# Performance work log

Measured on AMD Instinct MI355X. Metric: run time of the kernel, lower is better.

## Reference

```python
import jax, jax.numpy as jnp
import numpy as np

B, T_FRAMES, C, WS = 8, 8, 32, 128
N = 1024            # sample_size^2 points per frame
HW = WS * WS        # 16384 grid cells
BT = B * T_FRAMES


def setup_inputs() -> dict:
    key = jax.random.key(0)
    k1, k2, k3 = jax.random.split(key, 3)
    rng = np.random.default_rng(0)
    # per-frame grid-cell id for each of N points
    pose = rng.integers(0, HW, size=(BT, N))
    sorted_indices = np.argsort(pose, axis=1).astype(np.int32)
    sorted_pose = np.take_along_axis(pose, sorted_indices, axis=1)
    seq_unique_list = np.zeros((BT, N), dtype=np.int32)
    seq_unique_counts = np.zeros((BT, N), dtype=np.int32)
    for i in range(BT):
        u, c = np.unique(sorted_pose[i], return_counts=True)
        seq_unique_list[i, : len(u)] = u
        seq_unique_counts[i, : len(u)] = c
    return {
        "w_part": jax.random.normal(k1, (BT, N, C), dtype=jnp.float32),
        "sorted_indices": jnp.asarray(sorted_indices),
        "seq_unique_list": jnp.asarray(seq_unique_list),
        "seq_unique_counts": jnp.asarray(seq_unique_counts),
        "past_w": jax.random.normal(k2, (B, C, WS, WS), dtype=jnp.float32),
        "past_w_num_mask": jax.random.uniform(k3, (B, 1, WS, WS), dtype=jnp.float32) * 4.0,
        "T": T_FRAMES,
    }


def reference(w_part, sorted_indices, seq_unique_list, seq_unique_counts, past_w, past_w_num_mask, T):
    bt, n, c = w_part.shape
    b = bt // T
    ws = past_w.shape[2]
    hw = ws * ws
    # F.normalize(dim=-1), eps=1e-12
    wp = w_part / jnp.maximum(jnp.linalg.norm(w_part, axis=-1, keepdims=True), 1e-12)
    # gather: reorder points so same-cell points are contiguous
    gathered = jnp.take_along_axis(wp, sorted_indices[..., None].astype(jnp.int32), axis=1)  # (bt, n, c)
    counts = seq_unique_counts  # (bt, n) padded with zeros
    # segment id of each point from cumulative counts (points are sorted by cell)
    cum = jnp.cumsum(counts, axis=1)
    pt = jnp.arange(n)
    seg = jax.vmap(lambda cu: jnp.searchsorted(cu, pt, side='right'))(cum)  # (bt, n)
    sums = jax.vmap(lambda g, s: jax.ops.segment_sum(g, s, num_segments=n))(gathered, seg)  # (bt, n, c)
    means = sums / jnp.maximum(counts, 1)[..., None].astype(wp.dtype)
    # scatter means into dense grid; padded (count==0) slots routed out-of-bounds and dropped
    idx = jnp.where(counts > 0, seq_unique_list, hw)
    scat = jax.vmap(lambda m, i: jnp.zeros((hw, c), wp.dtype).at[i].set(m, mode='drop'))(means, idx)  # (bt, hw, c)
    mask = jax.vmap(lambda ct, i: jnp.zeros((hw,), wp.dtype).at[i].set(ct.astype(wp.dtype), mode='drop'))(counts, idx)
    new_w = scat.reshape(b, T, hw, c).mean(axis=1)                 # (b, hw, c)
    new_w = new_w.transpose(0, 2, 1).reshape(b, c, ws, ws)          # (b, c, ws, ws)
    w_num_mask = mask.reshape(b, T, hw).sum(axis=1).reshape(b, 1, ws, ws)
    # merge with past map; denominator is detached in the original
    new_w_num_mask = jax.lax.stop_gradient(w_num_mask) + jax.lax.stop_gradient(past_w_num_mask)
    new_w_num_mask = jnp.where(new_w_num_mask == 0, 1.0, new_w_num_mask)
    w = (new_w * w_num_mask + past_w * past_w_num_mask) / new_w_num_mask
    return w, new_w_num_mask
```

## Files before the change

kernel.cpp:

```cpp
#include <hip/hip_runtime.h>
#include <climits>

#define BATCH   8
#define TFRAMES 8
#define BT      (BATCH * TFRAMES)
#define NPTS    1024
#define NCH     32
#define WS      128
#define HW      (WS * WS)
#define CELLS   128
#define CHUNKS  (HW / CELLS)
#define CPAD    33

__global__ __launch_bounds__(256) void scan_kernel(
    const int* __restrict__ uniq_cnt,
    const int* __restrict__ uniq_list,
    int*       __restrict__ starts,
    int*       __restrict__ ranges)
{
    __shared__ int s_tot[256];
    __shared__ int s_key[NPTS];
    const int tid = threadIdx.x;
    const int bt  = blockIdx.x;

    const int4 c4 = reinterpret_cast<const int4*>(uniq_cnt + bt * NPTS)[tid];
    const int4 l4 = reinterpret_cast<const int4*>(uniq_list + bt * NPTS)[tid];
    s_key[tid * 4 + 0] = (c4.x > 0) ? l4.x : INT_MAX;
    s_key[tid * 4 + 1] = (c4.y > 0) ? l4.y : INT_MAX;
    s_key[tid * 4 + 2] = (c4.z > 0) ? l4.z : INT_MAX;
    s_key[tid * 4 + 3] = (c4.w > 0) ? l4.w : INT_MAX;

    const int l0 = c4.x;
    const int l1 = l0 + c4.y;
    const int l2 = l1 + c4.z;
    const int l3 = l2 + c4.w;
    s_tot[tid] = l3;
    __syncthreads();
    for (int off = 1; off < 256; off <<= 1) {
        int v = (tid >= off) ? s_tot[tid - off] : 0;
        __syncthreads();
        s_tot[tid] += v;
        __syncthreads();
    }
    const int ex = (tid > 0) ? s_tot[tid - 1] : 0;
    int4 st;
    st.x = ex;
    st.y = ex + l0;
    st.z = ex + l1;
    st.w = ex + l2;
    reinterpret_cast<int4*>(starts + bt * NPTS)[tid] = st;

    if (tid <= CHUNKS) {
        const int X = tid * CELLS;
        int lo = 0, hi = NPTS;
        while (lo < hi) {
            const int mid = (lo + hi) >> 1;
            if (s_key[mid] < X) lo = mid + 1; else hi = mid;
        }
        ranges[bt * (CHUNKS + 1) + tid] = lo;
    }
}

__global__ __launch_bounds__(256) void tile_kernel(
    const float* __restrict__ w_part,
    const int*   __restrict__ sorted_idx,
    const int*   __restrict__ uniq_list,
    const int*   __restrict__ uniq_cnt,
    const int*   __restrict__ starts,
    const int*   __restrict__ ranges,
    const float* __restrict__ past_w,
    const float* __restrict__ past_mask,
    float*       __restrict__ out_w,
    float*       __restrict__ out_mask)
{
    __shared__ float s_acc[CELLS][CPAD];
    __shared__ float s_mask[CELLS];

    const int tid      = threadIdx.x;
    const int b        = blockIdx.x / CHUNKS;
    const int chunk    = blockIdx.x % CHUNKS;
    const int cellBase = chunk * CELLS;

    float* flat = &s_acc[0][0];
    for (int i = tid; i < CELLS * CPAD; i += 256) flat[i] = 0.0f;
    if (tid < CELLS) s_mask[tid] = 0.0f;
    __syncthreads();

    const int wave  = tid >> 6;
    const int lane  = tid & 63;
    const int slot  = lane >> 3;
    const int lane8 = lane & 7;

    for (int tt = 0; tt < 2; ++tt) {
        const int t  = wave * 2 + tt;
        const int bt = b * TFRAMES + t;
        const int lo = ranges[bt * (CHUNKS + 1) + chunk];
        const int hi = ranges[bt * (CHUNKS + 1) + chunk + 1];
        const int* __restrict__ lst  = uniq_list + bt * NPTS;
        const int* __restrict__ cnts = uniq_cnt + bt * NPTS;
        const int* __restrict__ stp  = starts + bt * NPTS;
        const int* __restrict__ si   = sorted_idx + bt * NPTS;

        for (int e0 = lo; e0 < hi; e0 += 8) {
            const int e = e0 + slot;
            if (e < hi) {
                const int cell  = lst[e];
                const int cnt   = cnts[e];
                const int start = stp[e];
                float4 lacc = make_float4(0.f, 0.f, 0.f, 0.f);
                for (int p = start; p < start + cnt; ++p) {
                    const int j = si[p];
                    const float4 v = *reinterpret_cast<const float4*>(
                        w_part + ((size_t)bt * NPTS + j) * NCH + lane8 * 4);
                    float ss = v.x * v.x + v.y * v.y + v.z * v.z + v.w * v.w;
                    ss += __shfl_xor(ss, 1);
                    ss += __shfl_xor(ss, 2);
                    ss += __shfl_xor(ss, 4);
                    const float scale = 1.0f / fmaxf(sqrtf(ss), 1e-12f);
                    lacc.x += v.x * scale;
                    lacc.y += v.y * scale;
                    lacc.z += v.z * scale;
                    lacc.w += v.w * scale;
                }
                const float invc = 1.0f / (float)cnt;
                const int cl = cell - cellBase;
                float* ap = &s_acc[cl][lane8 * 4];
                atomicAdd(ap + 0, lacc.x * invc);
                atomicAdd(ap + 1, lacc.y * invc);
                atomicAdd(ap + 2, lacc.z * invc);
                atomicAdd(ap + 3, lacc.w * invc);
                if (lane8 == 0) atomicAdd(&s_mask[cl], (float)cnt);
            }
        }
    }
    __syncthreads();

    const int cellq = tid & 31;
    const int cgrp  = tid >> 5;
    const int c0    = cgrp * 4;
    const int gc    = cellBase + cellq * 4;
    const float invT = 1.0f / (float)TFRAMES;

    const float4 pm4 = *reinterpret_cast<const float4*>(past_mask + (size_t)b * HW + gc);
    float m[4], pm[4], r[4], dn[4];
    pm[0] = pm4.x; pm[1] = pm4.y; pm[2] = pm4.z; pm[3] = pm4.w;
#pragma unroll
    for (int i = 0; i < 4; ++i) {
        m[i] = s_mask[cellq * 4 + i];
        const float nwm = m[i] + pm[i];
        dn[i] = (nwm == 0.0f) ? 1.0f : nwm;
        r[i] = 1.0f / dn[i];
    }
    if (cgrp == 0) {
        float4 d4 = make_float4(dn[0], dn[1], dn[2], dn[3]);
        *reinterpret_cast<float4*>(out_mask + (size_t)b * HW + gc) = d4;
    }

#pragma unroll
    for (int k = 0; k < 4; ++k) {
        const int c = c0 + k;
        const size_t a = ((size_t)b * NCH + c) * HW + gc;
        const float4 pw = *reinterpret_cast<const float4*>(past_w + a);
        float4 o;
        o.x = (s_acc[cellq * 4 + 0][c] * invT * m[0] + pw.x * pm[0]) * r[0];
        o.y = (s_acc[cellq * 4 + 1][c] * invT * m[1] + pw.y * pm[1]) * r[1];
        o.z = (s_acc[cellq * 4 + 2][c] * invT * m[2] + pw.z * pm[2]) * r[2];
        o.w = (s_acc[cellq * 4 + 3][c] * invT * m[3] + pw.w * pm[3]) * r[3];
        *reinterpret_cast<float4*>(out_w + a) = o;
    }
}

extern "C" void kernel_launch(void* const* d_in, const int* in_sizes, int n_in,
                              void* d_out, int out_size, void* d_ws, size_t ws_size,
                              hipStream_t stream) {
    (void)in_sizes; (void)n_in; (void)out_size; (void)ws_size;

    const float* w_part     = (const float*)d_in[0];
    const int*   sorted_idx = (const int*)d_in[1];
    const int*   uniq_list  = (const int*)d_in[2];
    const int*   uniq_cnt   = (const int*)d_in[3];
    const float* past_w     = (const float*)d_in[4];
    const float* past_mask  = (const float*)d_in[5];

    float* out      = (float*)d_out;
    float* out_w    = out;
    float* out_mask = out + (size_t)BATCH * NCH * HW;

    int* starts = (int*)d_ws;
    int* ranges = starts + (size_t)BT * NPTS;

    scan_kernel<<<BT, 256, 0, stream>>>(uniq_cnt, uniq_list, starts, ranges);

    tile_kernel<<<BATCH * CHUNKS, 256, 0, stream>>>(
        w_part, sorted_idx, uniq_list, uniq_cnt, starts, ranges,
        past_w, past_mask, out_w, out_mask);
}
```

Before: 29.71 us.

## Pack segment metadata, use wave-shuffle scan, one frame per wave with 512 threads

The scan kernel now uses a wave-level shuffle scan instead of a shared-memory Hillis-Steele loop with many barriers. It writes cell, count and start as one packed int4 per segment, so the tile kernel does a single vector load per segment instead of three scattered int loads. The tile kernel doubles to 512 threads so each wave handles one frame instead of two. It also prefetches past_w and past_mask before the accumulation phase so that latency overlaps the gather work. The trade-offs are more workspace traffic (16 bytes per entry) and higher per-block register and thread pressure.

```diff
diff --git a/kernel.cpp b/kernel.cpp
--- a/kernel.cpp
+++ b/kernel.cpp
@@ -11,17 +11,21 @@
 #define CELLS   128
 #define CHUNKS  (HW / CELLS)
 #define CPAD    33
+#define TPB     512
 
 __global__ __launch_bounds__(256) void scan_kernel(
     const int* __restrict__ uniq_cnt,
     const int* __restrict__ uniq_list,
-    int*       __restrict__ starts,
+    int4*      __restrict__ entries,
     int*       __restrict__ ranges)
 {
-    __shared__ int s_tot[256];
     __shared__ int s_key[NPTS];
-    const int tid = threadIdx.x;
-    const int bt  = blockIdx.x;
+    __shared__ int s_wsum[4];
+
+    const int tid  = threadIdx.x;
+    const int bt   = blockIdx.x;
+    const int wave = tid >> 6;
+    const int lane = tid & 63;
 
     const int4 c4 = reinterpret_cast<const int4*>(uniq_cnt + bt * NPTS)[tid];
     const int4 l4 = reinterpret_cast<const int4*>(uniq_list + bt * NPTS)[tid];
@@ -30,25 +34,28 @@
     s_key[tid * 4 + 2] = (c4.z > 0) ? l4.z : INT_MAX;
     s_key[tid * 4 + 3] = (c4.w > 0) ? l4.w : INT_MAX;
 
-    const int l0 = c4.x;
-    const int l1 = l0 + c4.y;
-    const int l2 = l1 + c4.z;
-    const int l3 = l2 + c4.w;
-    s_tot[tid] = l3;
+    const int lsum = c4.x + c4.y + c4.z + c4.w;
+
+    int inc = lsum;
+#pragma unroll
+    for (int d = 1; d < 64; d <<= 1) {
+        const int v = __shfl_up(inc, d);
+        if (lane >= d) inc += v;
+    }
+    if (lane == 63) s_wsum[wave] = inc;
     __syncthreads();
-    for (int off = 1; off < 256; off <<= 1) {
-        int v = (tid >= off) ? s_tot[tid - off] : 0;
-        __syncthreads();
-        s_tot[tid] += v;
-        __syncthreads();
-    }
-    const int ex = (tid > 0) ? s_tot[tid - 1] : 0;
-    int4 st;
-    st.x = ex;
-    st.y = ex + l0;
-    st.z = ex + l1;
-    st.w = ex + l2;
-    reinterpret_cast<int4*>(starts + bt * NPTS)[tid] = st;
+
+    int woff = 0;
+#pragma unroll
+    for (int w = 0; w < 4; ++w)
+        if (w < wave) woff += s_wsum[w];
+
+    int st = woff + inc - lsum;
+    int4* ep = entries + (size_t)bt * NPTS + tid * 4;
+    ep[0] = make_int4(l4.x, c4.x, st, 0);             st += c4.x;
+    ep[1] = make_int4(l4.y, c4.y, st, 0);             st += c4.y;
+    ep[2] = make_int4(l4.z, c4.z, st, 0);             st += c4.z;
+    ep[3] = make_int4(l4.w, c4.w, st, 0);
 
     if (tid <= CHUNKS) {
         const int X = tid * CELLS;
@@ -61,12 +68,10 @@
     }
 }
 
-__global__ __launch_bounds__(256) void tile_kernel(
+__global__ __launch_bounds__(TPB) void tile_kernel(
     const float* __restrict__ w_part,
     const int*   __restrict__ sorted_idx,
-    const int*   __restrict__ uniq_list,
-    const int*   __restrict__ uniq_cnt,
-    const int*   __restrict__ starts,
+    const int4*  __restrict__ entries,
     const int*   __restrict__ ranges,
     const float* __restrict__ past_w,
     const float* __restrict__ past_mask,
@@ -81,8 +86,18 @@
     const int chunk    = blockIdx.x % CHUNKS;
     const int cellBase = chunk * CELLS;
 
+    const int cellq = tid & 31;
+    const int cgrp  = tid >> 5;
+    const int c0    = cgrp * 2;
+    const int gc    = cellBase + cellq * 4;
+    const size_t mbase = (size_t)b * HW + gc;
+    const float4 pm4 = *reinterpret_cast<const float4*>(past_mask + mbase);
+    const size_t a0 = ((size_t)b * NCH + c0) * HW + gc;
+    const float4 pw0 = *reinterpret_cast<const float4*>(past_w + a0);
+    const float4 pw1 = *reinterpret_cast<const float4*>(past_w + a0 + HW);
+
     float* flat = &s_acc[0][0];
-    for (int i = tid; i < CELLS * CPAD; i += 256) flat[i] = 0.0f;
+    for (int i = tid; i < CELLS * CPAD; i += TPB) flat[i] = 0.0f;
     if (tid < CELLS) s_mask[tid] = 0.0f;
     __syncthreads();
 
@@ -91,57 +106,48 @@
     const int slot  = lane >> 3;
     const int lane8 = lane & 7;
 
-    for (int tt = 0; tt < 2; ++tt) {
-        const int t  = wave * 2 + tt;
-        const int bt = b * TFRAMES + t;
-        const int lo = ranges[bt * (CHUNKS + 1) + chunk];
-        const int hi = ranges[bt * (CHUNKS + 1) + chunk + 1];
-        const int* __restrict__ lst  = uniq_list + bt * NPTS;
-        const int* __restrict__ cnts = uniq_cnt + bt * NPTS;
-        const int* __restrict__ stp  = starts + bt * NPTS;
-        const int* __restrict__ si   = sorted_idx + bt * NPTS;
-
-        for (int e0 = lo; e0 < hi; e0 += 8) {
-            const int e = e0 + slot;
-            if (e < hi) {
-                const int cell  = lst[e];
-                const int cnt   = cnts[e];
-                const int start = stp[e];
-                float4 lacc = make_float4(0.f, 0.f, 0.f, 0.f);
-                for (int p = start; p < start + cnt; ++p) {
-                    const int j = si[p];
-                    const float4 v = *reinterpret_cast<const float4*>(
-                        w_part + ((size_t)bt * NPTS + j) * NCH + lane8 * 4);
-                    float ss = v.x * v.x + v.y * v.y + v.z * v.z + v.w * v.w;
-                    ss += __shfl_xor(ss, 1);
-                    ss += __shfl_xor(ss, 2);
-                    ss += __shfl_xor(ss, 4);
-                    const float scale = 1.0f / fmaxf(sqrtf(ss), 1e-12f);
-                    lacc.x += v.x * scale;
-                    lacc.y += v.y * scale;
-                    lacc.z += v.z * scale;
-                    lacc.w += v.w * scale;
-                }
-                const float invc = 1.0f / (float)cnt;
-                const int cl = cell - cellBase;
-                float* ap = &s_acc[cl][lane8 * 4];
-                atomicAdd(ap + 0, lacc.x * invc);
-                atomicAdd(ap + 1, lacc.y * invc);
-                atomicAdd(ap + 2, lacc.z * invc);
-                atomicAdd(ap + 3, lacc.w * invc);
-                if (lane8 == 0) atomicAdd(&s_mask[cl], (float)cnt);
+    const int bt = b * TFRAMES + wave;
+    const int lo = ranges[bt * (CHUNKS + 1) + chunk];
+    const int hi = ranges[bt * (CHUNKS + 1) + chunk + 1];
+    const int4* __restrict__ ent = entries + (size_t)bt * NPTS;
+    const int*  __restrict__ si  = sorted_idx + bt * NPTS;
+    const float* __restrict__ wp = w_part + (size_t)bt * NPTS * NCH;
+
+    for (int e0 = lo; e0 < hi; e0 += 8) {
+        const int e = e0 + slot;
+        if (e < hi) {
+            const int4 meta = ent[e];
+            const int cell  = meta.x;
+            const int cnt   = meta.y;
+            const int start = meta.z;
+            float4 lacc = make_float4(0.f, 0.f, 0.f, 0.f);
+            for (int p = start; p < start + cnt; ++p) {
+                const int j = si[p];
+                const float4 v = *reinterpret_cast<const float4*>(
+                    wp + (size_t)j * NCH + lane8 * 4);
+                float ss = v.x * v.x + v.y * v.y + v.z * v.z + v.w * v.w;
+                ss += __shfl_xor(ss, 1);
+                ss += __shfl_xor(ss, 2);
+                ss += __shfl_xor(ss, 4);
+                const float scale = 1.0f / fmaxf(sqrtf(ss), 1e-12f);
+                lacc.x += v.x * scale;
+                lacc.y += v.y * scale;
+                lacc.z += v.z * scale;
+                lacc.w += v.w * scale;
             }
+            const float invc = 1.0f / (float)cnt;
+            const int cl = cell - cellBase;
+            float* ap = &s_acc[cl][lane8 * 4];
+            atomicAdd(ap + 0, lacc.x * invc);
+            atomicAdd(ap + 1, lacc.y * invc);
+            atomicAdd(ap + 2, lacc.z * invc);
+            atomicAdd(ap + 3, lacc.w * invc);
+            if (lane8 == 0) atomicAdd(&s_mask[cl], (float)cnt);
         }
     }
     __syncthreads();
 
-    const int cellq = tid & 31;
-    const int cgrp  = tid >> 5;
-    const int c0    = cgrp * 4;
-    const int gc    = cellBase + cellq * 4;
     const float invT = 1.0f / (float)TFRAMES;
-
-    const float4 pm4 = *reinterpret_cast<const float4*>(past_mask + (size_t)b * HW + gc);
     float m[4], pm[4], r[4], dn[4];
     pm[0] = pm4.x; pm[1] = pm4.y; pm[2] = pm4.z; pm[3] = pm4.w;
 #pragma unroll
@@ -152,22 +158,21 @@
         r[i] = 1.0f / dn[i];
     }
     if (cgrp == 0) {
-        float4 d4 = make_float4(dn[0], dn[1], dn[2], dn[3]);
-        *reinterpret_cast<float4*>(out_mask + (size_t)b * HW + gc) = d4;
-    }
-
-#pragma unroll
-    for (int k = 0; k < 4; ++k) {
-        const int c = c0 + k;
-        const size_t a = ((size_t)b * NCH + c) * HW + gc;
-        const float4 pw = *reinterpret_cast<const float4*>(past_w + a);
-        float4 o;
-        o.x = (s_acc[cellq * 4 + 0][c] * invT * m[0] + pw.x * pm[0]) * r[0];
-        o.y = (s_acc[cellq * 4 + 1][c] * invT * m[1] + pw.y * pm[1]) * r[1];
-        o.z = (s_acc[cellq * 4 + 2][c] * invT * m[2] + pw.z * pm[2]) * r[2];
-        o.w = (s_acc[cellq * 4 + 3][c] * invT * m[3] + pw.w * pm[3]) * r[3];
-        *reinterpret_cast<float4*>(out_w + a) = o;
-    }
+        *reinterpret_cast<float4*>(out_mask + mbase) =
+            make_float4(dn[0], dn[1], dn[2], dn[3]);
+    }
+
+    float4 o0, o1;
+    o0.x = (s_acc[cellq * 4 + 0][c0] * invT * m[0] + pw0.x * pm[0]) * r[0];
+    o0.y = (s_acc[cellq * 4 + 1][c0] * invT * m[1] + pw0.y * pm[1]) * r[1];
+    o0.z = (s_acc[cellq * 4 + 2][c0] * invT * m[2] + pw0.z * pm[2]) * r[2];
+    o0.w = (s_acc[cellq * 4 + 3][c0] * invT * m[3] + pw0.w * pm[3]) * r[3];
+    o1.x = (s_acc[cellq * 4 + 0][c0 + 1] * invT * m[0] + pw1.x * pm[0]) * r[0];
+    o1.y = (s_acc[cellq * 4 + 1][c0 + 1] * invT * m[1] + pw1.y * pm[1]) * r[1];
+    o1.z = (s_acc[cellq * 4 + 2][c0 + 1] * invT * m[2] + pw1.z * pm[2]) * r[2];
+    o1.w = (s_acc[cellq * 4 + 3][c0 + 1] * invT * m[3] + pw1.w * pm[3]) * r[3];
+    *reinterpret_cast<float4*>(out_w + a0)      = o0;
+    *reinterpret_cast<float4*>(out_w + a0 + HW) = o1;
 }
 
 extern "C" void kernel_launch(void* const* d_in, const int* in_sizes, int n_in,
@@ -186,12 +191,12 @@
     float* out_w    = out;
     float* out_mask = out + (size_t)BATCH * NCH * HW;
 
-    int* starts = (int*)d_ws;
-    int* ranges = starts + (size_t)BT * NPTS;
-
-    scan_kernel<<<BT, 256, 0, stream>>>(uniq_cnt, uniq_list, starts, ranges);
-
-    tile_kernel<<<BATCH * CHUNKS, 256, 0, stream>>>(
-        w_part, sorted_idx, uniq_list, uniq_cnt, starts, ranges,
+    int4* entries = (int4*)d_ws;
+    int*  ranges  = (int*)(entries + (size_t)BT * NPTS);
+
+    scan_kernel<<<BT, 256, 0, stream>>>(uniq_cnt, uniq_list, entries, ranges);
+
+    tile_kernel<<<BATCH * CHUNKS, TPB, 0, stream>>>(
+        w_part, sorted_idx, entries, ranges,
         past_w, past_mask, out_w, out_mask);
 }
```

New measurement: 30.03 us. About the same (+1.1%).
